# Optimization experiments

Measured on AMD Instinct MI355X. Metric: run time of the kernel, lower is better.

Reference implementation:

```python
import jax, jax.numpy as jnp
import numpy as np

TEMPERATURE = 0.07
BASE_TEMPERATURE = 0.07
N_CLASSES = 360


def setup_inputs() -> dict:
    key = jax.random.key(0)
    k1, k2 = jax.random.split(key)
    B, D = 8192, 256
    features = jax.random.normal(k1, (B, D), dtype=jnp.float32)
    labels = jax.random.randint(k2, (B,), 0, N_CLASSES, dtype=jnp.int64)
    sigma = jnp.ones((1,), dtype=jnp.float32)
    return {"features": features, "labels": labels, "sigma": sigma}


def reference(features, labels, sigma):
    B = features.shape[0]
    labels = labels.reshape(-1, 1)
    # pairwise positive mask [B, B]
    mask = (labels == labels.T).astype(jnp.float32)
    # negated scaled dot products [B, B]
    anchor_dot_contrast = -(features @ features.T) / TEMPERATURE
    logits_max = jax.lax.stop_gradient(jnp.max(anchor_dot_contrast, axis=1, keepdims=True))
    logits = anchor_dot_contrast - logits_max
    # remove self-pairs
    logits_mask = 1.0 - jnp.eye(B, dtype=jnp.float32)
    mask = mask * logits_mask
    exp_logits = jnp.exp(logits)
    negative_mask = logits_mask - mask
    negative_counts = jnp.sum(negative_mask, axis=1, keepdims=True)
    mean_exp_negatives = jnp.sum(exp_logits * negative_mask, axis=1, keepdims=True) / (negative_counts + 1e-8)
    exp_positives_sum = jnp.sum(exp_logits * mask, axis=1, keepdims=True)
    denominator = exp_positives_sum + mean_exp_negatives
    log_prob = logits - jnp.log(denominator)
    mask_pos_pairs = jnp.sum(mask, axis=1)
    mask_pos_pairs = jnp.where(mask_pos_pairs < 1e-6, 1.0, mask_pos_pairs)
    mean_log_prob_pos = jnp.sum(mask * log_prob, axis=1) / mask_pos_pairs
    loss = (TEMPERATURE / BASE_TEMPERATURE) * mean_log_prob_pos
    return jnp.mean(loss)
```

## Files before the change

### kernel.cpp

```cpp
#include <hip/hip_runtime.h>
#include <hip/hip_bf16.h>
#include <math.h>

typedef unsigned int u32;
typedef unsigned short u16;
typedef __bf16 bf16_t;
typedef bf16_t bf16x8 __attribute__((ext_vector_type(8)));
typedef float f32x4 __attribute__((ext_vector_type(4)));

#define B_N 8192
#define D_K 256
#define NCLS 360
#define BM 128
#define BN 64
#define NSPLIT 8
#define COLS (B_N / NSPLIT)
#define NT (COLS / BN)
#define MAXC 61

#define SCALE2 (-20.609929155556627f)
#define LN2 (0.6931471805599453f)
#define INV_T (14.285714285714286f)

__device__ __forceinline__ float fexp2(float x) { return __builtin_amdgcn_exp2f(x); }

__device__ __forceinline__ u16 f2bf(float x) {
  u32 u = __float_as_uint(x);
  u32 r = (u + 0x7fffu + ((u >> 16) & 1u)) >> 16;
  return (u16)r;
}

__device__ __forceinline__ void gl_lds16(const void* g, void* l) {
  __builtin_amdgcn_global_load_lds(
      (const __attribute__((address_space(1))) u32*)g,
      (__attribute__((address_space(3))) u32*)l, 16, 0, 0);
}

__global__ void k_prep(const float* __restrict__ f, u16* __restrict__ fbf,
                       float* __restrict__ out) {
  if (blockIdx.x == 0 && threadIdx.x == 0) out[0] = 0.f;
  int t = blockIdx.x * 256 + threadIdx.x;
  int e4 = t * 4;
  const float4 v = *reinterpret_cast<const float4*>(f + e4);
  ushort4 b;
  b.x = f2bf(v.x); b.y = f2bf(v.y); b.z = f2bf(v.z); b.w = f2bf(v.w);
  *reinterpret_cast<ushort4*>(fbf + e4) = b;
}

__global__ __launch_bounds__(256, 2) void k_main(const u16* __restrict__ fb,
                                                 float2* __restrict__ part) {
  __shared__ __align__(16) u16 Bs[2][BN * D_K];

  const int tid = threadIdx.x;
  const int lane = tid & 63;
  const int w = tid >> 6;
  const int t15 = lane & 15;
  const int g = lane >> 4;
  const int t7 = t15 & 7;
  const int rb = blockIdx.x & 63;
  const int sp = blockIdx.x >> 6;
  const int rowbase = rb * BM + w * 32;
  const int colbase = sp * COLS;

  bf16x8 A[2][8];
#pragma unroll
  for (int rs = 0; rs < 2; ++rs)
#pragma unroll
    for (int kk = 0; kk < 8; ++kk) {
      const u16* p = fb + (size_t)(rowbase + rs * 16 + t15) * D_K + kk * 32 + g * 8;
      A[rs][kk] = *reinterpret_cast<const bf16x8*>(p);
    }

  const u16* srcp[8];
  u16* dstp[8];
#pragma unroll
  for (int it = 0; it < 8; ++it) {
    int lin = (w * 8 + it) * 1024 + lane * 16;
    int row = lin >> 9;
    int c = (lin >> 4) & 31;
    int q = c ^ (row & 7);
    srcp[it] = fb + (size_t)(colbase + row) * D_K + q * 8;
    dstp[it] = &Bs[0][0] + (w * 8 + it) * 512;
  }

  const int gl = g ^ (t7 & 3);
  const int b2 = (t7 >> 2) & 1;
  const int offE = t15 * 256 + b2 * 32 + gl * 8;
  const int offO = t15 * 256 + (b2 ^ 1) * 32 + gl * 8;

  float m2[8], Ea[8];
#pragma unroll
  for (int i = 0; i < 8; ++i) { m2[i] = -1e30f; Ea[i] = 0.f; }

#pragma unroll
  for (int it = 0; it < 8; ++it) gl_lds16(srcp[it], dstp[it]);
  __syncthreads();

  const f32x4 z4 = {0.f, 0.f, 0.f, 0.f};
  for (int t = 0; t < NT; ++t) {
    if (t + 1 < NT) {
      const int soff = (t + 1) * (BN * D_K);
      const int doff = ((t + 1) & 1) * (BN * D_K / 4);
#pragma unroll
      for (int it = 0; it < 8; ++it) gl_lds16(srcp[it] + soff, dstp[it] + doff * 4);
    }

    const u16* bufp = &Bs[t & 1][0];
    const u16* beE = bufp + offE;
    const u16* beO = bufp + offO;

    f32x4 C[2][4];
#pragma unroll
    for (int kk = 0; kk < 8; ++kk) {
      bf16x8 Bf[4];
#pragma unroll
      for (int s = 0; s < 4; ++s) {
        const u16* ba = (kk & 1) ? beO : beE;
        Bf[s] = *reinterpret_cast<const bf16x8*>(ba + (kk >> 1) * 64 + s * 4096);
      }
#pragma unroll
      for (int rs = 0; rs < 2; ++rs)
#pragma unroll
        for (int s = 0; s < 4; ++s)
          C[rs][s] = __builtin_amdgcn_mfma_f32_16x16x32_bf16(
              A[rs][kk], Bf[s], (kk == 0) ? z4 : C[rs][s], 0, 0, 0);
    }

#pragma unroll
    for (int rs = 0; rs < 2; ++rs) {
#pragma unroll
      for (int q = 0; q < 4; ++q) {
        const int slot = rs * 4 + q;
        float c0 = C[rs][0][q], c1 = C[rs][1][q];
        float c2 = C[rs][2][q], c3 = C[rs][3][q];
        float tm = fminf(fminf(c0, c1), fminf(c2, c3));
        float nm = fmaxf(m2[slot], tm * SCALE2);
        float sc = fexp2(m2[slot] - nm);
        float e0 = fexp2(fmaf(c0, SCALE2, -nm));
        float e1 = fexp2(fmaf(c1, SCALE2, -nm));
        float e2 = fexp2(fmaf(c2, SCALE2, -nm));
        float e3 = fexp2(fmaf(c3, SCALE2, -nm));
        Ea[slot] = fmaf(Ea[slot], sc, (e0 + e1) + (e2 + e3));
        m2[slot] = nm;
      }
    }
    __syncthreads();
  }

#pragma unroll
  for (int st = 1; st < 16; st <<= 1) {
#pragma unroll
    for (int i = 0; i < 8; ++i) {
      float om = __shfl_xor(m2[i], st);
      float oa = __shfl_xor(Ea[i], st);
      float nm = fmaxf(m2[i], om);
      Ea[i] = Ea[i] * fexp2(m2[i] - nm) + oa * fexp2(om - nm);
      m2[i] = nm;
    }
  }
  if (t15 == 0) {
#pragma unroll
    for (int rs = 0; rs < 2; ++rs)
#pragma unroll
      for (int q = 0; q < 4; ++q) {
        int row = rowbase + rs * 16 + g * 4 + q;
        part[sp * B_N + row] = make_float2(m2[rs * 4 + q], Ea[rs * 4 + q]);
      }
  }
}

__global__ __launch_bounds__(256) void k_final(const float* __restrict__ f,
                                               const int* __restrict__ lab,
                                               const float2* __restrict__ part,
                                               float* __restrict__ out) {
  __shared__ __align__(16) float4 feat[MAXC][65];
  __shared__ float m2a[MAXC], Eaa[MAXC], Epa[MAXC], sda[MAXC];
  __shared__ int idx[MAXC];
  __shared__ int nS;
  const int c = blockIdx.x;
  const int tid = threadIdx.x;
  const int lane = tid & 63;
  const int w = tid >> 6;
  if (tid == 0) nS = 0;
  __syncthreads();

  for (int i = tid; i < B_N / 4; i += 256) {
    const int4 lv = reinterpret_cast<const int4*>(lab)[i];
    if (lv.x == c) { int p = atomicAdd(&nS, 1); if (p < MAXC) idx[p] = i * 4 + 0; }
    if (lv.y == c) { int p = atomicAdd(&nS, 1); if (p < MAXC) idx[p] = i * 4 + 1; }
    if (lv.z == c) { int p = atomicAdd(&nS, 1); if (p < MAXC) idx[p] = i * 4 + 2; }
    if (lv.w == c) { int p = atomicAdd(&nS, 1); if (p < MAXC) idx[p] = i * 4 + 3; }
  }
  __syncthreads();
  const int n = nS < MAXC ? nS : MAXC;

  for (int j = w; j < n; j += 4)
    feat[j][lane] = reinterpret_cast<const float4*>(f + (size_t)idx[j] * D_K)[lane];

  for (int j = w; j < n; j += 4) {
    float m2 = -1e30f, Ea = 0.f;
    if (lane < NSPLIT) {
      float2 p = part[lane * B_N + idx[j]];
      m2 = p.x; Ea = p.y;
    }
#pragma unroll
    for (int st = 1; st < NSPLIT; st <<= 1) {
      float om = __shfl_xor(m2, st);
      float oa = __shfl_xor(Ea, st);
      float nm = fmaxf(m2, om);
      Ea = Ea * fexp2(m2 - nm) + oa * fexp2(om - nm);
      m2 = nm;
    }
    if (lane == 0) { m2a[j] = m2; Eaa[j] = Ea; Epa[j] = 0.f; sda[j] = 0.f; }
  }
  __syncthreads();

  const int ntile = (n + 7) >> 3;
  const int jj = lane >> 3, kk = lane & 7;
  for (int tile = w; tile < ntile * ntile; tile += 4) {
    const int j = (tile / ntile) * 8 + jj;
    const int k = (tile % ntile) * 8 + kk;
    const bool ok = (j < n) && (k < n) && (j != k);
    const int jc = j < n ? j : 0, kc = k < n ? k : 0;
    f32x4 acc = {0.f, 0.f, 0.f, 0.f};
#pragma unroll 8
    for (int d = 0; d < 64; ++d) {
      const float4 a = feat[jc][d];
      const float4 b = feat[kc][d];
      acc[0] = fmaf(a.x, b.x, acc[0]);
      acc[1] = fmaf(a.y, b.y, acc[1]);
      acc[2] = fmaf(a.z, b.z, acc[2]);
      acc[3] = fmaf(a.w, b.w, acc[3]);
    }
    float dot = ok ? ((acc[0] + acc[1]) + (acc[2] + acc[3])) : 0.f;
    float ex = ok ? fexp2(fmaf(dot, SCALE2, -m2a[jc])) : 0.f;
#pragma unroll
    for (int st = 1; st < 8; st <<= 1) {
      dot += __shfl_xor(dot, st);
      ex += __shfl_xor(ex, st);
    }
    if (kk == 0 && j < n) {
      atomicAdd(&sda[j], dot);
      atomicAdd(&Epa[j], ex);
    }
  }
  __syncthreads();

  if (w == 0) {
    float contrib = 0.f;
    if (lane < n) {
      const int j = lane;
      float m2 = m2a[j], Ea = Eaa[j], Ep = Epa[j], sumdot = sda[j];
      float En = fmaxf(Ea - Ep, 0.f);
      int cntp = n - 1;
      float cntn = (float)(B_N - 1 - cntp);
      float denom = Ep + En / (cntn + 1e-8f);
      float Sadc = -sumdot * INV_T;
      float num = Sadc - (float)cntp * (m2 * LN2) - (float)cntp * logf(denom);
      float dv = (cntp <= 0) ? 1.f : (float)cntp;
      contrib = num / dv;
    }
#pragma unroll
    for (int st = 1; st < 64; st <<= 1) contrib += __shfl_xor(contrib, st);
    if (lane == 0) atomicAdd(out, contrib * (1.f / (float)B_N));
  }
}

extern "C" void kernel_launch(void* const* d_in, const int* in_sizes, int n_in,
                              void* d_out, int out_size, void* d_ws, size_t ws_size,
                              hipStream_t stream) {
  const float* f = (const float*)d_in[0];
  const int* lab = (const int*)d_in[1];

  char* ws = (char*)d_ws;
  u16* fbf = (u16*)ws;
  float2* part = (float2*)(ws + 4194304);

  k_prep<<<2048, 256, 0, stream>>>(f, fbf, (float*)d_out);
  k_main<<<64 * NSPLIT, 256, 0, stream>>>(fbf, part);
  k_final<<<NCLS, 256, 0, stream>>>(f, lab, part, (float*)d_out);
}
```

Baseline: 69.47 us.

## Exploit Gram matrix symmetry with upper-triangular 128x128 tile grid

Replaces the row-block by column-split loop with one block per upper-triangular 128x128 tile of the symmetric Gram matrix (2080 blocks). Each block produces per-row partial logsumexp stats and, for off-diagonal tiles, per-column stats written to the transposed partition, so nearly half the matmul work is skipped. The final kernel now merges 64 partials per row instead of 8. The cost is more partial-buffer traffic, extra cross-lane and LDS reductions for the column stats, and no load/compute pipelining inside a block.

```diff
diff --git a/kernel.cpp b/kernel.cpp
--- a/kernel.cpp
+++ b/kernel.cpp
@@ -11,11 +11,9 @@
 #define B_N 8192
 #define D_K 256
 #define NCLS 360
-#define BM 128
-#define BN 64
-#define NSPLIT 8
-#define COLS (B_N / NSPLIT)
-#define NT (COLS / BN)
+#define NG 64
+#define NBLK 2080
+#define NPART 64
 #define MAXC 61
 
 #define SCALE2 (-20.609929155556627f)
@@ -49,7 +47,8 @@
 
 __global__ __launch_bounds__(256, 2) void k_main(const u16* __restrict__ fb,
                                                  float2* __restrict__ part) {
-  __shared__ __align__(16) u16 Bs[2][BN * D_K];
+  __shared__ __align__(16) u16 Bs[128 * D_K];
+  __shared__ float2 colred[4][128];
 
   const int tid = threadIdx.x;
   const int lane = tid & 63;
@@ -57,10 +56,25 @@
   const int t15 = lane & 15;
   const int g = lane >> 4;
   const int t7 = t15 & 7;
-  const int rb = blockIdx.x & 63;
-  const int sp = blockIdx.x >> 6;
-  const int rowbase = rb * BM + w * 32;
-  const int colbase = sp * COLS;
+
+  const int bid = blockIdx.x;
+#define TRI(x) ((x) * NG - ((x) * ((x)-1)) / 2)
+  int i = (int)((129.0 - sqrt(129.0 * 129.0 - 8.0 * (double)bid)) * 0.5);
+  i = i < 0 ? 0 : (i > NG - 1 ? NG - 1 : i);
+  while (TRI(i + 1) <= bid) ++i;
+  while (TRI(i) > bid) --i;
+  const int j = i + (bid - TRI(i));
+  const int rowbase = i * 128 + w * 32;
+  const int colb = j * 128;
+
+#pragma unroll
+  for (int it = 0; it < 16; ++it) {
+    int lin = (w * 16 + it) * 1024 + lane * 16;
+    int row = lin >> 9;
+    int c = (lin >> 4) & 31;
+    int q = c ^ (row & 7);
+    gl_lds16(fb + (size_t)(colb + row) * D_K + q * 8, &Bs[0] + (w * 16 + it) * 512);
+  }
 
   bf16x8 A[2][8];
 #pragma unroll
@@ -71,101 +85,87 @@
       A[rs][kk] = *reinterpret_cast<const bf16x8*>(p);
     }
 
-  const u16* srcp[8];
-  u16* dstp[8];
-#pragma unroll
-  for (int it = 0; it < 8; ++it) {
-    int lin = (w * 8 + it) * 1024 + lane * 16;
-    int row = lin >> 9;
-    int c = (lin >> 4) & 31;
-    int q = c ^ (row & 7);
-    srcp[it] = fb + (size_t)(colbase + row) * D_K + q * 8;
-    dstp[it] = &Bs[0][0] + (w * 8 + it) * 512;
-  }
-
-  const int gl = g ^ (t7 & 3);
+  __syncthreads();
+
+  const int gl8 = (g ^ (t7 & 3)) * 8;
   const int b2 = (t7 >> 2) & 1;
-  const int offE = t15 * 256 + b2 * 32 + gl * 8;
-  const int offO = t15 * 256 + (b2 ^ 1) * 32 + gl * 8;
-
-  float m2[8], Ea[8];
-#pragma unroll
-  for (int i = 0; i < 8; ++i) { m2[i] = -1e30f; Ea[i] = 0.f; }
-
-#pragma unroll
-  for (int it = 0; it < 8; ++it) gl_lds16(srcp[it], dstp[it]);
-  __syncthreads();
+  const int offE = t15 * 256 + gl8 + b2 * 32;
+  const int offO = t15 * 256 + gl8 + (b2 ^ 1) * 32;
 
   const f32x4 z4 = {0.f, 0.f, 0.f, 0.f};
-  for (int t = 0; t < NT; ++t) {
-    if (t + 1 < NT) {
-      const int soff = (t + 1) * (BN * D_K);
-      const int doff = ((t + 1) & 1) * (BN * D_K / 4);
-#pragma unroll
-      for (int it = 0; it < 8; ++it) gl_lds16(srcp[it] + soff, dstp[it] + doff * 4);
-    }
-
-    const u16* bufp = &Bs[t & 1][0];
-    const u16* beE = bufp + offE;
-    const u16* beO = bufp + offO;
-
-    f32x4 C[2][4];
-#pragma unroll
-    for (int kk = 0; kk < 8; ++kk) {
-      bf16x8 Bf[4];
-#pragma unroll
-      for (int s = 0; s < 4; ++s) {
-        const u16* ba = (kk & 1) ? beO : beE;
-        Bf[s] = *reinterpret_cast<const bf16x8*>(ba + (kk >> 1) * 64 + s * 4096);
+  f32x4 C[2][8];
+#pragma unroll
+  for (int kk = 0; kk < 8; ++kk) {
+    bf16x8 Bf[8];
+    const u16* ba = &Bs[0] + ((kk & 1) ? offO : offE) + (kk >> 1) * 64;
+#pragma unroll
+    for (int s = 0; s < 8; ++s)
+      Bf[s] = *reinterpret_cast<const bf16x8*>(ba + s * 4096);
+#pragma unroll
+    for (int rs = 0; rs < 2; ++rs)
+#pragma unroll
+      for (int s = 0; s < 8; ++s)
+        C[rs][s] = __builtin_amdgcn_mfma_f32_16x16x32_bf16(
+            A[rs][kk], Bf[s], (kk == 0) ? z4 : C[rs][s], 0, 0, 0);
+  }
+
+#pragma unroll
+  for (int rs = 0; rs < 2; ++rs) {
+#pragma unroll
+    for (int q = 0; q < 4; ++q) {
+      float v0 = C[rs][0][q], v1 = C[rs][1][q], v2 = C[rs][2][q], v3 = C[rs][3][q];
+      float v4 = C[rs][4][q], v5 = C[rs][5][q], v6 = C[rs][6][q], v7 = C[rs][7][q];
+      float m = fminf(fminf(fminf(v0, v1), fminf(v2, v3)),
+                      fminf(fminf(v4, v5), fminf(v6, v7)));
+      float mL = m * SCALE2;
+      float e = ((fexp2(fmaf(v0, SCALE2, -mL)) + fexp2(fmaf(v1, SCALE2, -mL))) +
+                 (fexp2(fmaf(v2, SCALE2, -mL)) + fexp2(fmaf(v3, SCALE2, -mL)))) +
+                ((fexp2(fmaf(v4, SCALE2, -mL)) + fexp2(fmaf(v5, SCALE2, -mL))) +
+                 (fexp2(fmaf(v6, SCALE2, -mL)) + fexp2(fmaf(v7, SCALE2, -mL))));
+#pragma unroll
+      for (int st = 1; st < 16; st <<= 1) {
+        float om = __shfl_xor(mL, st);
+        float oe = __shfl_xor(e, st);
+        float nm = fmaxf(mL, om);
+        e = e * fexp2(mL - nm) + oe * fexp2(om - nm);
+        mL = nm;
       }
-#pragma unroll
-      for (int rs = 0; rs < 2; ++rs)
-#pragma unroll
-        for (int s = 0; s < 4; ++s)
-          C[rs][s] = __builtin_amdgcn_mfma_f32_16x16x32_bf16(
-              A[rs][kk], Bf[s], (kk == 0) ? z4 : C[rs][s], 0, 0, 0);
-    }
-
-#pragma unroll
-    for (int rs = 0; rs < 2; ++rs) {
-#pragma unroll
-      for (int q = 0; q < 4; ++q) {
-        const int slot = rs * 4 + q;
-        float c0 = C[rs][0][q], c1 = C[rs][1][q];
-        float c2 = C[rs][2][q], c3 = C[rs][3][q];
-        float tm = fminf(fminf(c0, c1), fminf(c2, c3));
-        float nm = fmaxf(m2[slot], tm * SCALE2);
-        float sc = fexp2(m2[slot] - nm);
-        float e0 = fexp2(fmaf(c0, SCALE2, -nm));
-        float e1 = fexp2(fmaf(c1, SCALE2, -nm));
-        float e2 = fexp2(fmaf(c2, SCALE2, -nm));
-        float e3 = fexp2(fmaf(c3, SCALE2, -nm));
-        Ea[slot] = fmaf(Ea[slot], sc, (e0 + e1) + (e2 + e3));
-        m2[slot] = nm;
+      if (t15 == 0)
+        part[(size_t)j * B_N + rowbase + rs * 16 + g * 4 + q] = make_float2(mL, e);
+    }
+  }
+
+  if (i != j) {
+#pragma unroll
+    for (int s = 0; s < 8; ++s) {
+      float v0 = C[0][s][0], v1 = C[0][s][1], v2 = C[0][s][2], v3 = C[0][s][3];
+      float v4 = C[1][s][0], v5 = C[1][s][1], v6 = C[1][s][2], v7 = C[1][s][3];
+      float m = fminf(fminf(fminf(v0, v1), fminf(v2, v3)),
+                      fminf(fminf(v4, v5), fminf(v6, v7)));
+      m = fminf(m, __shfl_xor(m, 16));
+      m = fminf(m, __shfl_xor(m, 32));
+      float mL = m * SCALE2;
+      float e = ((fexp2(fmaf(v0, SCALE2, -mL)) + fexp2(fmaf(v1, SCALE2, -mL))) +
+                 (fexp2(fmaf(v2, SCALE2, -mL)) + fexp2(fmaf(v3, SCALE2, -mL)))) +
+                ((fexp2(fmaf(v4, SCALE2, -mL)) + fexp2(fmaf(v5, SCALE2, -mL))) +
+                 (fexp2(fmaf(v6, SCALE2, -mL)) + fexp2(fmaf(v7, SCALE2, -mL))));
+      e += __shfl_xor(e, 16);
+      e += __shfl_xor(e, 32);
+      if (g == 0) colred[w][s * 16 + t15] = make_float2(mL, e);
+    }
+    __syncthreads();
+    if (tid < 128) {
+      float2 p = colred[0][tid];
+      float m = p.x, e = p.y;
+#pragma unroll
+      for (int ww = 1; ww < 4; ++ww) {
+        float2 o = colred[ww][tid];
+        float nm = fmaxf(m, o.x);
+        e = e * fexp2(m - nm) + o.y * fexp2(o.x - nm);
+        m = nm;
       }
-    }
-    __syncthreads();
-  }
-
-#pragma unroll
-  for (int st = 1; st < 16; st <<= 1) {
-#pragma unroll
-    for (int i = 0; i < 8; ++i) {
-      float om = __shfl_xor(m2[i], st);
-      float oa = __shfl_xor(Ea[i], st);
-      float nm = fmaxf(m2[i], om);
-      Ea[i] = Ea[i] * fexp2(m2[i] - nm) + oa * fexp2(om - nm);
-      m2[i] = nm;
-    }
-  }
-  if (t15 == 0) {
-#pragma unroll
-    for (int rs = 0; rs < 2; ++rs)
-#pragma unroll
-      for (int q = 0; q < 4; ++q) {
-        int row = rowbase + rs * 16 + g * 4 + q;
-        part[sp * B_N + row] = make_float2(m2[rs * 4 + q], Ea[rs * 4 + q]);
-      }
+      part[(size_t)i * B_N + colb + tid] = make_float2(m, e);
+    }
   }
 }
 
@@ -198,13 +198,10 @@
     feat[j][lane] = reinterpret_cast<const float4*>(f + (size_t)idx[j] * D_K)[lane];
 
   for (int j = w; j < n; j += 4) {
-    float m2 = -1e30f, Ea = 0.f;
-    if (lane < NSPLIT) {
-      float2 p = part[lane * B_N + idx[j]];
-      m2 = p.x; Ea = p.y;
-    }
-#pragma unroll
-    for (int st = 1; st < NSPLIT; st <<= 1) {
+    float2 p = part[(size_t)lane * B_N + idx[j]];
+    float m2 = p.x, Ea = p.y;
+#pragma unroll
+    for (int st = 1; st < NPART; st <<= 1) {
       float om = __shfl_xor(m2, st);
       float oa = __shfl_xor(Ea, st);
       float nm = fmaxf(m2, om);
@@ -277,6 +274,6 @@
   float2* part = (float2*)(ws + 4194304);
 
   k_prep<<<2048, 256, 0, stream>>>(f, fbf, (float*)d_out);
-  k_main<<<64 * NSPLIT, 256, 0, stream>>>(fbf, part);
+  k_main<<<NBLK, 256, 0, stream>>>(fbf, part);
   k_final<<<NCLS, 256, 0, stream>>>(f, lab, part, (float*)d_out);
 }
```

New measurement: 83.72 us. 20.5% more time.

## Exploit Gram matrix symmetry by computing only upper-triangular tiles with column reductions

Applied to the files above, without the earlier changes.

The main GEMM kernel now walks only the upper-triangular block region of the symmetric feature Gram matrix. Each off-diagonal tile also feeds a per-column online log-sum-exp reduction, so the transposed rows get their partials without recomputing the tile. This roughly halves the MFMA and load work. In exchange it adds column-side exp work, shuffles, an LDS reduction and extra partial slots that k_final must merge per row, and some blocks do fewer tiles than others.

```diff
diff --git a/kernel.cpp b/kernel.cpp
--- a/kernel.cpp
+++ b/kernel.cpp
@@ -11,11 +11,7 @@
 #define B_N 8192
 #define D_K 256
 #define NCLS 360
-#define BM 128
-#define BN 64
-#define NSPLIT 8
-#define COLS (B_N / NSPLIT)
-#define NT (COLS / BN)
+#define NBLK 544
 #define MAXC 61
 
 #define SCALE2 (-20.609929155556627f)
@@ -49,7 +45,8 @@
 
 __global__ __launch_bounds__(256, 2) void k_main(const u16* __restrict__ fb,
                                                  float2* __restrict__ part) {
-  __shared__ __align__(16) u16 Bs[2][BN * D_K];
+  __shared__ __align__(16) u16 Bs[2][16384];
+  __shared__ float2 colred[2][4][64];
 
   const int tid = threadIdx.x;
   const int lane = tid & 63;
@@ -57,10 +54,19 @@
   const int t15 = lane & 15;
   const int g = lane >> 4;
   const int t7 = t15 & 7;
-  const int rb = blockIdx.x & 63;
-  const int sp = blockIdx.x >> 6;
-  const int rowbase = rb * BM + w * 32;
-  const int colbase = sp * COLS;
+
+  const int bid = blockIdx.x;
+  int i = 0, cum = 0;
+  for (;;) {
+    int ci = (135 - 2 * i) >> 3;
+    if (bid < cum + ci) break;
+    cum += ci; ++i;
+  }
+  const int kc = bid - cum;
+  const int jc0 = 2 * i + kc * 8;
+  const int nt = (128 - jc0) < 8 ? (128 - jc0) : 8;
+  const int col0 = jc0 * 64;
+  const int rowbase = i * 128 + w * 32;
 
   bf16x8 A[2][8];
 #pragma unroll
@@ -79,30 +85,30 @@
     int row = lin >> 9;
     int c = (lin >> 4) & 31;
     int q = c ^ (row & 7);
-    srcp[it] = fb + (size_t)(colbase + row) * D_K + q * 8;
+    srcp[it] = fb + (size_t)(col0 + row) * D_K + q * 8;
     dstp[it] = &Bs[0][0] + (w * 8 + it) * 512;
   }
 
-  const int gl = g ^ (t7 & 3);
+  const int gl8 = (g ^ (t7 & 3)) * 8;
   const int b2 = (t7 >> 2) & 1;
-  const int offE = t15 * 256 + b2 * 32 + gl * 8;
-  const int offO = t15 * 256 + (b2 ^ 1) * 32 + gl * 8;
+  const int offE = t15 * 256 + gl8 + b2 * 32;
+  const int offO = t15 * 256 + gl8 + (b2 ^ 1) * 32;
 
   float m2[8], Ea[8];
 #pragma unroll
-  for (int i = 0; i < 8; ++i) { m2[i] = -1e30f; Ea[i] = 0.f; }
+  for (int s = 0; s < 8; ++s) { m2[s] = -1e30f; Ea[s] = 0.f; }
 
 #pragma unroll
   for (int it = 0; it < 8; ++it) gl_lds16(srcp[it], dstp[it]);
   __syncthreads();
 
   const f32x4 z4 = {0.f, 0.f, 0.f, 0.f};
-  for (int t = 0; t < NT; ++t) {
-    if (t + 1 < NT) {
-      const int soff = (t + 1) * (BN * D_K);
-      const int doff = ((t + 1) & 1) * (BN * D_K / 4);
-#pragma unroll
-      for (int it = 0; it < 8; ++it) gl_lds16(srcp[it] + soff, dstp[it] + doff * 4);
+  for (int t = 0; t < nt; ++t) {
+    if (t + 1 < nt) {
+      const int soff = (t + 1) * 16384;
+      const int doff = ((t + 1) & 1) * 16384;
+#pragma unroll
+      for (int it = 0; it < 8; ++it) gl_lds16(srcp[it] + soff, dstp[it] + doff);
     }
 
     const u16* bufp = &Bs[t & 1][0];
@@ -144,18 +150,52 @@
         m2[slot] = nm;
       }
     }
+
+    const int jc = jc0 + t;
+    const bool docol = (jc >> 1) != i;
+    if (docol) {
+#pragma unroll
+      for (int s = 0; s < 4; ++s) {
+        float v0 = C[0][s][0], v1 = C[0][s][1], v2 = C[0][s][2], v3 = C[0][s][3];
+        float v4 = C[1][s][0], v5 = C[1][s][1], v6 = C[1][s][2], v7 = C[1][s][3];
+        float m = fminf(fminf(fminf(v0, v1), fminf(v2, v3)),
+                        fminf(fminf(v4, v5), fminf(v6, v7)));
+        m = fminf(m, __shfl_xor(m, 16));
+        m = fminf(m, __shfl_xor(m, 32));
+        float mL = m * SCALE2;
+        float e = ((fexp2(fmaf(v0, SCALE2, -mL)) + fexp2(fmaf(v1, SCALE2, -mL))) +
+                   (fexp2(fmaf(v2, SCALE2, -mL)) + fexp2(fmaf(v3, SCALE2, -mL)))) +
+                  ((fexp2(fmaf(v4, SCALE2, -mL)) + fexp2(fmaf(v5, SCALE2, -mL))) +
+                   (fexp2(fmaf(v6, SCALE2, -mL)) + fexp2(fmaf(v7, SCALE2, -mL))));
+        e += __shfl_xor(e, 16);
+        e += __shfl_xor(e, 32);
+        if (g == 0) colred[t & 1][w][s * 16 + t15] = make_float2(mL, e);
+      }
+    }
     __syncthreads();
+    if (docol && tid < 64) {
+      float2 p = colred[t & 1][0][tid];
+      float m = p.x, e = p.y;
+#pragma unroll
+      for (int ww = 1; ww < 4; ++ww) {
+        float2 o = colred[t & 1][ww][tid];
+        float nm = fmaxf(m, o.x);
+        e = e * fexp2(m - nm) + o.y * fexp2(o.x - nm);
+        m = nm;
+      }
+      part[(size_t)i * B_N + jc * 64 + tid] = make_float2(m, e);
+    }
   }
 
 #pragma unroll
   for (int st = 1; st < 16; st <<= 1) {
 #pragma unroll
-    for (int i = 0; i < 8; ++i) {
-      float om = __shfl_xor(m2[i], st);
-      float oa = __shfl_xor(Ea[i], st);
-      float nm = fmaxf(m2[i], om);
-      Ea[i] = Ea[i] * fexp2(m2[i] - nm) + oa * fexp2(om - nm);
-      m2[i] = nm;
+    for (int s = 0; s < 8; ++s) {
+      float om = __shfl_xor(m2[s], st);
+      float oa = __shfl_xor(Ea[s], st);
+      float nm = fmaxf(m2[s], om);
+      Ea[s] = Ea[s] * fexp2(m2[s] - nm) + oa * fexp2(om - nm);
+      m2[s] = nm;
     }
   }
   if (t15 == 0) {
@@ -164,7 +204,8 @@
 #pragma unroll
       for (int q = 0; q < 4; ++q) {
         int row = rowbase + rs * 16 + g * 4 + q;
-        part[sp * B_N + row] = make_float2(m2[rs * 4 + q], Ea[rs * 4 + q]);
+        part[(size_t)(i + kc) * B_N + row] =
+            make_float2(m2[rs * 4 + q], Ea[rs * 4 + q]);
       }
   }
 }
@@ -198,13 +239,16 @@
     feat[j][lane] = reinterpret_cast<const float4*>(f + (size_t)idx[j] * D_K)[lane];
 
   for (int j = w; j < n; j += 4) {
+    const int r = idx[j];
+    const int jr = r >> 7;
+    const int cnt = jr + ((135 - 2 * jr) >> 3);
     float m2 = -1e30f, Ea = 0.f;
-    if (lane < NSPLIT) {
-      float2 p = part[lane * B_N + idx[j]];
+    if (lane < cnt) {
+      float2 p = part[(size_t)lane * B_N + r];
       m2 = p.x; Ea = p.y;
     }
 #pragma unroll
-    for (int st = 1; st < NSPLIT; st <<= 1) {
+    for (int st = 1; st < 64; st <<= 1) {
       float om = __shfl_xor(m2, st);
       float oa = __shfl_xor(Ea, st);
       float nm = fmaxf(m2, om);
@@ -221,12 +265,12 @@
     const int j = (tile / ntile) * 8 + jj;
     const int k = (tile % ntile) * 8 + kk;
     const bool ok = (j < n) && (k < n) && (j != k);
-    const int jc = j < n ? j : 0, kc = k < n ? k : 0;
+    const int jc = j < n ? j : 0, kcc = k < n ? k : 0;
     f32x4 acc = {0.f, 0.f, 0.f, 0.f};
 #pragma unroll 8
     for (int d = 0; d < 64; ++d) {
       const float4 a = feat[jc][d];
-      const float4 b = feat[kc][d];
+      const float4 b = feat[kcc][d];
       acc[0] = fmaf(a.x, b.x, acc[0]);
       acc[1] = fmaf(a.y, b.y, acc[1]);
       acc[2] = fmaf(a.z, b.z, acc[2]);
@@ -277,6 +321,6 @@
   float2* part = (float2*)(ws + 4194304);
 
   k_prep<<<2048, 256, 0, stream>>>(f, fbf, (float*)d_out);
-  k_main<<<64 * NSPLIT, 256, 0, stream>>>(fbf, part);
+  k_main<<<NBLK, 256, 0, stream>>>(fbf, part);
   k_final<<<NCLS, 256, 0, stream>>>(f, lab, part, (float*)d_out);
 }
```

Result: slower. 84.74 us (+22.0%).

## Fuse bf16 conversion into main kernel, loading fp32 features directly

Applied to the files above, without the earlier changes.

Drops the separate bf16 prep kernel. The main kernel now reads fp32 features, converts them to bf16 in registers and stores them to LDS. The direct global-to-LDS loads are replaced by register-staged prefetch: loads are issued before the MFMA and softmax work and written to LDS after it. This saves a launch and the bf16 round trip through memory, but doubles global read bytes per tile, re-converts each tile in every block, and raises register pressure.

```diff
diff --git a/kernel.cpp b/kernel.cpp
--- a/kernel.cpp
+++ b/kernel.cpp
@@ -24,34 +24,20 @@
 
 __device__ __forceinline__ float fexp2(float x) { return __builtin_amdgcn_exp2f(x); }
 
-__device__ __forceinline__ u16 f2bf(float x) {
-  u32 u = __float_as_uint(x);
-  u32 r = (u + 0x7fffu + ((u >> 16) & 1u)) >> 16;
-  return (u16)r;
-}
-
-__device__ __forceinline__ void gl_lds16(const void* g, void* l) {
-  __builtin_amdgcn_global_load_lds(
-      (const __attribute__((address_space(1))) u32*)g,
-      (__attribute__((address_space(3))) u32*)l, 16, 0, 0);
-}
-
-__global__ void k_prep(const float* __restrict__ f, u16* __restrict__ fbf,
-                       float* __restrict__ out) {
-  if (blockIdx.x == 0 && threadIdx.x == 0) out[0] = 0.f;
-  int t = blockIdx.x * 256 + threadIdx.x;
-  int e4 = t * 4;
-  const float4 v = *reinterpret_cast<const float4*>(f + e4);
-  ushort4 b;
-  b.x = f2bf(v.x); b.y = f2bf(v.y); b.z = f2bf(v.z); b.w = f2bf(v.w);
-  *reinterpret_cast<ushort4*>(fbf + e4) = b;
-}
-
-__global__ __launch_bounds__(256, 2) void k_main(const u16* __restrict__ fb,
-                                                 float2* __restrict__ part) {
-  __shared__ __align__(16) u16 Bs[2][BN * D_K];
+__device__ __forceinline__ bf16x8 pack8(float4 a, float4 b) {
+  bf16x8 v;
+  v[0] = (bf16_t)a.x; v[1] = (bf16_t)a.y; v[2] = (bf16_t)a.z; v[3] = (bf16_t)a.w;
+  v[4] = (bf16_t)b.x; v[5] = (bf16_t)b.y; v[6] = (bf16_t)b.z; v[7] = (bf16_t)b.w;
+  return v;
+}
+
+__global__ __launch_bounds__(256, 2) void k_main(const float* __restrict__ f,
+                                                 float2* __restrict__ part,
+                                                 float* __restrict__ out) {
+  __shared__ __align__(16) u16 Bs[2][16384];
 
   const int tid = threadIdx.x;
+  if (blockIdx.x == 0 && tid == 0) out[0] = 0.f;
   const int lane = tid & 63;
   const int w = tid >> 6;
   const int t15 = lane & 15;
@@ -67,43 +53,56 @@
   for (int rs = 0; rs < 2; ++rs)
 #pragma unroll
     for (int kk = 0; kk < 8; ++kk) {
-      const u16* p = fb + (size_t)(rowbase + rs * 16 + t15) * D_K + kk * 32 + g * 8;
-      A[rs][kk] = *reinterpret_cast<const bf16x8*>(p);
-    }
-
-  const u16* srcp[8];
-  u16* dstp[8];
+      const float4* pf = reinterpret_cast<const float4*>(
+          f + (size_t)(rowbase + rs * 16 + t15) * D_K + kk * 32 + g * 8);
+      A[rs][kk] = pack8(pf[0], pf[1]);
+    }
+
+  const float* sgp[8];
+  u16* sdp[8];
 #pragma unroll
   for (int it = 0; it < 8; ++it) {
     int lin = (w * 8 + it) * 1024 + lane * 16;
     int row = lin >> 9;
     int c = (lin >> 4) & 31;
     int q = c ^ (row & 7);
-    srcp[it] = fb + (size_t)(colbase + row) * D_K + q * 8;
-    dstp[it] = &Bs[0][0] + (w * 8 + it) * 512;
-  }
-
-  const int gl = g ^ (t7 & 3);
+    sgp[it] = f + (size_t)(colbase + row) * D_K + c * 8;
+    sdp[it] = &Bs[0][0] + row * 256 + q * 8;
+  }
+
+  const int gl8 = (g ^ (t7 & 3)) * 8;
   const int b2 = (t7 >> 2) & 1;
-  const int offE = t15 * 256 + b2 * 32 + gl * 8;
-  const int offO = t15 * 256 + (b2 ^ 1) * 32 + gl * 8;
+  const int offE = t15 * 256 + gl8 + b2 * 32;
+  const int offO = t15 * 256 + gl8 + (b2 ^ 1) * 32;
 
   float m2[8], Ea[8];
 #pragma unroll
   for (int i = 0; i < 8; ++i) { m2[i] = -1e30f; Ea[i] = 0.f; }
 
-#pragma unroll
-  for (int it = 0; it < 8; ++it) gl_lds16(srcp[it], dstp[it]);
+  float4 ra[8], rv[8];
+#define SLOAD(t)                                                               \
+  {                                                                            \
+    const int soff = (t) * (BN * D_K);                                         \
+    _Pragma("unroll") for (int it = 0; it < 8; ++it) {                         \
+      const float4* p4 = reinterpret_cast<const float4*>(sgp[it] + soff);      \
+      ra[it] = p4[0];                                                          \
+      rv[it] = p4[1];                                                          \
+    }                                                                          \
+  }
+#define SWRITE(t)                                                              \
+  {                                                                            \
+    const int doff = ((t) & 1) * 16384;                                        \
+    _Pragma("unroll") for (int it = 0; it < 8; ++it)                           \
+        *reinterpret_cast<bf16x8*>(sdp[it] + doff) = pack8(ra[it], rv[it]);    \
+  }
+
+  SLOAD(0);
+  SWRITE(0);
   __syncthreads();
 
   const f32x4 z4 = {0.f, 0.f, 0.f, 0.f};
   for (int t = 0; t < NT; ++t) {
-    if (t + 1 < NT) {
-      const int soff = (t + 1) * (BN * D_K);
-      const int doff = ((t + 1) & 1) * (BN * D_K / 4);
-#pragma unroll
-      for (int it = 0; it < 8; ++it) gl_lds16(srcp[it] + soff, dstp[it] + doff * 4);
-    }
+    if (t + 1 < NT) SLOAD(t + 1);
 
     const u16* bufp = &Bs[t & 1][0];
     const u16* beE = bufp + offE;
@@ -144,6 +143,8 @@
         m2[slot] = nm;
       }
     }
+
+    if (t + 1 < NT) SWRITE(t + 1);
     __syncthreads();
   }
 
@@ -272,11 +273,8 @@
   const float* f = (const float*)d_in[0];
   const int* lab = (const int*)d_in[1];
 
-  char* ws = (char*)d_ws;
-  u16* fbf = (u16*)ws;
-  float2* part = (float2*)(ws + 4194304);
-
-  k_prep<<<2048, 256, 0, stream>>>(f, fbf, (float*)d_out);
-  k_main<<<64 * NSPLIT, 256, 0, stream>>>(fbf, part);
+  float2* part = (float2*)d_ws;
+
+  k_main<<<64 * NSPLIT, 256, 0, stream>>>(f, part, (float*)d_out);
   k_final<<<NCLS, 256, 0, stream>>>(f, lab, part, (float*)d_out);
 }
```

Result: slower. 77.23 us (+11.2%).
